# Kernel tuning notes

Measured on AMD Instinct MI355X. Metric: run time of the kernel, lower is better.

The kernel has to match this reference:

```python
import jax, jax.numpy as jnp
import numpy as np

DT = 0.001          # continuous-dynamics step (dt > 0 branch)
KERNEL_SIZE = 16384 # L
P, H = 1024, 256    # d_state, d_input (= d_output)


def setup_inputs() -> dict:
    key = jax.random.key(0)
    kAr, kAi, kB, kC = jax.random.split(key, 4)
    # Continuous diagonal state matrix: real part in [strong, weak] = [-0.5, -0.01] (stable),
    # imaginary part uniform in [-pi, pi] (mimics diagonal_state_space_matrix init).
    Ar = jax.random.uniform(kAr, (P,), minval=-0.5, maxval=-0.01)
    Ai = jax.random.uniform(kAi, (P,), minval=-np.pi, maxval=np.pi)
    A = jnp.stack([Ar, Ai], axis=-1).astype(jnp.float32)            # (P, 2) view_as_real
    # B, C ~ uniform disk (radius 1): scaled complex gaussians are a fine stand-in numerically.
    B = (jax.random.normal(kB, (P, H, 2)) / np.sqrt(H)).astype(jnp.float32)   # (P, H, 2)
    C = (jax.random.normal(kC, (H, P, 2)) / np.sqrt(P)).astype(jnp.float32)   # (H, P, 2)
    return {"A": A, "B": B, "C": C}


def _as_complex(x):
    return x[..., 0] + 1j * x[..., 1]


def reference(A, B, C):
    """Vandermonde SSM kernel generation (continuous dt > 0 branch).
    Returns kernel (H, L, 2) = real view of complex kernel (H, L)."""
    Ac = _as_complex(A)   # (P,) complex
    Bc = _as_complex(B)   # (P, H)
    Cc = _as_complex(C)   # (H, P)

    # ZOH-style discretization
    A_bar = jnp.exp(Ac * DT)                               # (P,)
    B_bar = ((A_bar - 1.0) / Ac)[:, None] * Bc             # (P, H)

    # Vandermonde matrix V[p, l] = A_bar[p] ** l  (complex power == exp(l * log(a)))
    powers = jnp.arange(KERNEL_SIZE, dtype=jnp.float32)    # (L,)
    V = jnp.exp(jnp.log(A_bar)[:, None] * powers[None, :]) # (P, L)

    # W[h, p] = C[h, p] * B_bar[p, h]; kernel[h, l] = sum_p W[h, p] * V[p, l]
    W = Cc * B_bar.T                                       # (H, P)
    kernel = jnp.einsum('hp,pl->hl', W, V)                 # (H, L) complex
    return jnp.stack([kernel.real, kernel.imag], axis=-1)  # (H, L, 2) float32
```

## Files before the change

kernel.cpp:

```cpp
#include <hip/hip_runtime.h>
#include <hip/hip_fp16.h>

#define P_DIM 1024
#define H_DIM 256
#define L_DIM 16384
#define DT 0.001f
#define TWOPI 6.283185307179586f
#define INV2PI 0.15915494309189535f
#define WSCALE 4096.0f
#define INV_WSCALE (1.0f / 4096.0f)
#define BM 128
#define BN 128
#define BK 64
#define NT 256

typedef _Float16 f16x8 __attribute__((ext_vector_type(8)));
typedef float f32x4 __attribute__((ext_vector_type(4)));

#define GPTR(p) (const __attribute__((address_space(1))) unsigned*)(p)
#define LPTR(p) (__attribute__((address_space(3))) unsigned*)(p)

union H2U { __half2 h; unsigned u; };

__device__ __forceinline__ float2 cmulf(float2 a, float2 b) {
    return make_float2(a.x * b.x - a.y * b.y, a.x * b.y + a.y * b.x);
}

__global__ __launch_bounds__(256)
void prep_kernel(const float* __restrict__ Ag, const float* __restrict__ Bg,
                 const float* __restrict__ Cg, __half* __restrict__ W2) {
    __shared__ float2 Bt[64][33];
    __shared__ float2 sc[64];
    const int t  = threadIdx.x;
    const int p0 = (blockIdx.x & 15) << 6;
    const int h0 = (blockIdx.x >> 4) << 5;

    if (t < 64) {
        float2 a = ((const float2*)Ag)[p0 + t];
        float er = __expf(a.x * DT);
        float s, c; __sincosf(a.y * DT, &s, &c);
        float nr = er * c - 1.f, ni = er * s;
        float inv = 1.f / (a.x * a.x + a.y * a.y);
        sc[t] = make_float2((nr * a.x + ni * a.y) * inv, (ni * a.x - nr * a.y) * inv);
    }
    #pragma unroll
    for (int i = 0; i < 8; ++i) {
        int idx = i * 256 + t, p = idx >> 5, h = idx & 31;
        Bt[p][h] = ((const float2*)Bg)[(size_t)(p0 + p) * H_DIM + h0 + h];
    }
    __syncthreads();
    #pragma unroll
    for (int i = 0; i < 8; ++i) {
        int idx = i * 256 + t, h = idx >> 6, p = idx & 63;
        float2 cc = ((const float2*)Cg)[(size_t)(h0 + h) * P_DIM + p0 + p];
        float2 s2 = sc[p], b = Bt[p][h0 ? h : h];
        float2 tv = cmulf(cc, s2);
        float wr = (tv.x * b.x - tv.y * b.y) * WSCALE;
        float wi = (tv.x * b.y + tv.y * b.x) * WSCALE;
        ((__half2*)W2)[(size_t)(h0 + h) * P_DIM + p0 + p] =
            __float22half2_rn(make_float2(wr, wi));
    }
}

__global__ __launch_bounds__(NT, 2)
void vand_mfma_kernel(const float* __restrict__ Ag,
                      const _Float16* __restrict__ W2,
                      float* __restrict__ out) {
    __shared__ __attribute__((aligned(16))) _Float16 As[2][BM * BK];
    __shared__ __attribute__((aligned(16))) _Float16 Bs[2][BN * BK];

    const int tid  = threadIdx.x;
    const int lane = tid & 63;
    const int w    = tid >> 6;
    const int wm   = w & 1, wn = w >> 1;
    const int m0   = blockIdx.y * BM;
    const int nb   = blockIdx.x * BN;
    const int lb   = blockIdx.x * (BN / 2);

    const float2* Ag2 = (const float2*)Ag;

    f32x4 acc[4][4];
    #pragma unroll
    for (int mt = 0; mt < 4; ++mt)
        #pragma unroll
        for (int nt = 0; nt < 4; ++nt)
            acc[mt][nt] = (f32x4){0.f, 0.f, 0.f, 0.f};

    const int q    = tid & 15;
    const int llq  = (tid >> 4) << 2;
    const float l0f = (float)(lb + llq);
    const int grp  = q >> 1, sub = (q & 1) << 2;

    const int goff = (lane >> 3) * 2048 + (((lane & 7) ^ (lane >> 3)) << 3);
    const _Float16* gwbase = W2 + (size_t)(m0 + (w << 5)) * 2048;
    const int ldsoff = (w << 5) * 64;

    _Float16* Acur = &As[0][0]; _Float16* Bcur = &Bs[0][0];
    _Float16* Anxt = &As[1][0]; _Float16* Bnxt = &Bs[1][0];

#define DMA_CHUNK(K0, DST)                                                        \
    {                                                                             \
        const _Float16* gw = gwbase + (K0) + goff;                                \
        _Float16* lB = (DST) + ldsoff;                                            \
        _Pragma("unroll")                                                         \
        for (int r = 0; r < 4; ++r)                                               \
            __builtin_amdgcn_global_load_lds(GPTR(gw + r * 8 * 2048),             \
                                             LPTR(lB + r * 8 * 64), 16, 0, 0);    \
    }

#define VGEN_CHUNK(K0, DST)                                                       \
    {                                                                             \
        float2 a0 = Ag2[((K0) >> 1) + 2 * q];                                     \
        float2 a1 = Ag2[((K0) >> 1) + 2 * q + 1];                                 \
        float c0x = a0.x * DT, c0y = a0.y * (DT * INV2PI);                        \
        float c1x = a1.x * DT, c1y = a1.y * (DT * INV2PI);                        \
        float s, c;                                                               \
        float e0 = __expf(c0x); __sincosf(c0y * TWOPI, &s, &c);                   \
        float2 ab0 = make_float2(e0 * c, e0 * s);                                 \
        float e1 = __expf(c1x); __sincosf(c1y * TWOPI, &s, &c);                   \
        float2 ab1 = make_float2(e1 * c, e1 * s);                                 \
        float mg = __expf(c0x * l0f);                                             \
        float x = c0y * l0f; x -= rintf(x); __sincosf(x * TWOPI, &s, &c);         \
        float2 v0 = make_float2(mg * c, mg * s);                                  \
        mg = __expf(c1x * l0f);                                                   \
        x = c1y * l0f; x -= rintf(x); __sincosf(x * TWOPI, &s, &c);               \
        float2 v1 = make_float2(mg * c, mg * s);                                  \
        _Pragma("unroll")                                                         \
        for (int j = 0; j < 4; ++j) {                                             \
            int n0 = 2 * (llq + j);                                               \
            H2U h0u, h1u, h2u, h3u;                                               \
            h0u.h = __float22half2_rn(make_float2(v0.x, -v0.y));                  \
            h1u.h = __float22half2_rn(make_float2(v1.x, -v1.y));                  \
            h2u.h = __float22half2_rn(make_float2(v0.y, v0.x));                   \
            h3u.h = __float22half2_rn(make_float2(v1.y, v1.x));                   \
            int e0i = n0 * 64 + ((grp ^ (n0 & 7)) << 3) + sub;                    \
            int e1i = (n0 + 1) * 64 + ((grp ^ ((n0 + 1) & 7)) << 3) + sub;        \
            *(uint2*)((DST) + e0i) = make_uint2(h0u.u, h1u.u);                    \
            *(uint2*)((DST) + e1i) = make_uint2(h2u.u, h3u.u);                    \
            if (j < 3) { v0 = cmulf(v0, ab0); v1 = cmulf(v1, ab1); }              \
        }                                                                         \
    }

    DMA_CHUNK(0, Acur)
    VGEN_CHUNK(0, Bcur)
    __syncthreads();

    for (int kk = 0; kk < 32; ++kk) {
        if (kk < 31) {
            const int k1 = (kk + 1) * BK;
            DMA_CHUNK(k1, Anxt)
            VGEN_CHUNK(k1, Bnxt)
        }
        #pragma unroll
        for (int ks = 0; ks < 2; ++ks) {
            f16x8 af[4], bf[4];
            const int g = ks * 4 + (lane >> 4);
            #pragma unroll
            for (int t = 0; t < 4; ++t) {
                int m = wm * 64 + t * 16 + (lane & 15);
                af[t] = *(const f16x8*)(Acur + m * 64 + ((g ^ (m & 7)) << 3));
                int n = wn * 64 + t * 16 + (lane & 15);
                bf[t] = *(const f16x8*)(Bcur + n * 64 + ((g ^ (n & 7)) << 3));
            }
            #pragma unroll
            for (int mt = 0; mt < 4; ++mt)
                #pragma unroll
                for (int nt = 0; nt < 4; ++nt)
                    acc[mt][nt] = __builtin_amdgcn_mfma_f32_16x16x32_f16(
                        af[mt], bf[nt], acc[mt][nt], 0, 0, 0);
        }
        __syncthreads();
        _Float16* tA = Acur; Acur = Anxt; Anxt = tA;
        _Float16* tB = Bcur; Bcur = Bnxt; Bnxt = tB;
    }

    #pragma unroll
    for (int mt = 0; mt < 4; ++mt) {
        #pragma unroll
        for (int nt = 0; nt < 4; ++nt) {
            int h = m0 + wm * 64 + mt * 16 + ((lane >> 4) << 2);
            int n = nb + wn * 64 + nt * 16 + (lane & 15);
            #pragma unroll
            for (int r = 0; r < 4; ++r)
                out[(size_t)(h + r) * 32768 + n] = acc[mt][nt][r] * INV_WSCALE;
        }
    }
#undef DMA_CHUNK
#undef VGEN_CHUNK
}

extern "C" void kernel_launch(void* const* d_in, const int* in_sizes, int n_in,
                              void* d_out, int out_size, void* d_ws, size_t ws_size,
                              hipStream_t stream) {
    const float* A = (const float*)d_in[0];
    const float* B = (const float*)d_in[1];
    const float* C = (const float*)d_in[2];
    float* out = (float*)d_out;
    __half* W2 = (__half*)d_ws;

    prep_kernel<<<dim3(128), dim3(256), 0, stream>>>(A, B, C, W2);
    vand_mfma_kernel<<<dim3(L_DIM * 2 / BN, H_DIM / BM), dim3(NT), 0, stream>>>(
        A, (const _Float16*)W2, out);
}
```

Before: 111.7 us.

## Precompute discretized A table in LDS and regenerate Vandermonde tile with padded layout

The discretized A_bar values are now computed once per block into a shared-memory table, so each Vandermonde chunk no longer recomputes exp/sincos for the step factor. Thread mapping changes so each thread handles one state pair over 8 consecutive positions, halving the per-chunk transcendental starting-point evaluations. The B tile switches from XOR swizzle to a padded row stride with 4-byte stores. In exchange, the longer recurrence chain of 7 complex multiplies adds fp16 error and extra LDS, and the padded layout may bring bank conflicts on the stores.

Result: no change. 109.6 us (-1.9%).

```diff
diff --git a/kernel.cpp b/kernel.cpp
--- a/kernel.cpp
+++ b/kernel.cpp
@@ -13,6 +13,7 @@
 #define BN 128
 #define BK 64
 #define NT 256
+#define LDB 72
 
 typedef _Float16 f16x8 __attribute__((ext_vector_type(8)));
 typedef float f32x4 __attribute__((ext_vector_type(4)));
@@ -53,7 +54,7 @@
     for (int i = 0; i < 8; ++i) {
         int idx = i * 256 + t, h = idx >> 6, p = idx & 63;
         float2 cc = ((const float2*)Cg)[(size_t)(h0 + h) * P_DIM + p0 + p];
-        float2 s2 = sc[p], b = Bt[p][h0 ? h : h];
+        float2 s2 = sc[p], b = Bt[p][h];
         float2 tv = cmulf(cc, s2);
         float wr = (tv.x * b.x - tv.y * b.y) * WSCALE;
         float wi = (tv.x * b.y + tv.y * b.x) * WSCALE;
@@ -67,7 +68,8 @@
                       const _Float16* __restrict__ W2,
                       float* __restrict__ out) {
     __shared__ __attribute__((aligned(16))) _Float16 As[2][BM * BK];
-    __shared__ __attribute__((aligned(16))) _Float16 Bs[2][BN * BK];
+    __shared__ __attribute__((aligned(16))) _Float16 Bs[2][BN * LDB];
+    __shared__ float2 Atab[P_DIM];
 
     const int tid  = threadIdx.x;
     const int lane = tid & 63;
@@ -79,6 +81,15 @@
 
     const float2* Ag2 = (const float2*)Ag;
 
+    #pragma unroll
+    for (int i = 0; i < 4; ++i) {
+        int p = tid + i * 256;
+        float2 a = Ag2[p];
+        float e = __expf(a.x * DT);
+        float s, c; __sincosf(a.y * DT, &s, &c);
+        Atab[p] = make_float2(e * c, e * s);
+    }
+
     f32x4 acc[4][4];
     #pragma unroll
     for (int mt = 0; mt < 4; ++mt)
@@ -86,10 +97,10 @@
         for (int nt = 0; nt < 4; ++nt)
             acc[mt][nt] = (f32x4){0.f, 0.f, 0.f, 0.f};
 
-    const int q    = tid & 15;
-    const int llq  = (tid >> 4) << 2;
-    const float l0f = (float)(lb + llq);
-    const int grp  = q >> 1, sub = (q & 1) << 2;
+    const int pl    = tid & 31;
+    const int lg    = tid >> 5;
+    const float l0f = (float)(lb + lg * 8);
+    const int bpbase = lg * 16 * LDB + 2 * pl;
 
     const int goff = (lane >> 3) * 2048 + (((lane & 7) ^ (lane >> 3)) << 3);
     const _Float16* gwbase = W2 + (size_t)(m0 + (w << 5)) * 2048;
@@ -110,37 +121,27 @@
 
 #define VGEN_CHUNK(K0, DST)                                                       \
     {                                                                             \
-        float2 a0 = Ag2[((K0) >> 1) + 2 * q];                                     \
-        float2 a1 = Ag2[((K0) >> 1) + 2 * q + 1];                                 \
-        float c0x = a0.x * DT, c0y = a0.y * (DT * INV2PI);                        \
-        float c1x = a1.x * DT, c1y = a1.y * (DT * INV2PI);                        \
-        float s, c;                                                               \
-        float e0 = __expf(c0x); __sincosf(c0y * TWOPI, &s, &c);                   \
-        float2 ab0 = make_float2(e0 * c, e0 * s);                                 \
-        float e1 = __expf(c1x); __sincosf(c1y * TWOPI, &s, &c);                   \
-        float2 ab1 = make_float2(e1 * c, e1 * s);                                 \
-        float mg = __expf(c0x * l0f);                                             \
-        float x = c0y * l0f; x -= rintf(x); __sincosf(x * TWOPI, &s, &c);         \
-        float2 v0 = make_float2(mg * c, mg * s);                                  \
-        mg = __expf(c1x * l0f);                                                   \
-        x = c1y * l0f; x -= rintf(x); __sincosf(x * TWOPI, &s, &c);               \
-        float2 v1 = make_float2(mg * c, mg * s);                                  \
+        const int pg = ((K0) >> 1) + pl;                                          \
+        float2 a  = Ag2[pg];                                                      \
+        float2 ab = Atab[pg];                                                     \
+        float cx = a.x * DT, cy = a.y * (DT * INV2PI);                            \
+        float mg = __expf(cx * l0f);                                              \
+        float x  = cy * l0f; x -= rintf(x);                                       \
+        float s, c; __sincosf(x * TWOPI, &s, &c);                                 \
+        float2 v = make_float2(mg * c, mg * s);                                   \
+        _Float16* bp = (DST) + bpbase;                                            \
         _Pragma("unroll")                                                         \
-        for (int j = 0; j < 4; ++j) {                                             \
-            int n0 = 2 * (llq + j);                                               \
-            H2U h0u, h1u, h2u, h3u;                                               \
-            h0u.h = __float22half2_rn(make_float2(v0.x, -v0.y));                  \
-            h1u.h = __float22half2_rn(make_float2(v1.x, -v1.y));                  \
-            h2u.h = __float22half2_rn(make_float2(v0.y, v0.x));                   \
-            h3u.h = __float22half2_rn(make_float2(v1.y, v1.x));                   \
-            int e0i = n0 * 64 + ((grp ^ (n0 & 7)) << 3) + sub;                    \
-            int e1i = (n0 + 1) * 64 + ((grp ^ ((n0 + 1) & 7)) << 3) + sub;        \
-            *(uint2*)((DST) + e0i) = make_uint2(h0u.u, h1u.u);                    \
-            *(uint2*)((DST) + e1i) = make_uint2(h2u.u, h3u.u);                    \
-            if (j < 3) { v0 = cmulf(v0, ab0); v1 = cmulf(v1, ab1); }              \
+        for (int j = 0; j < 8; ++j) {                                             \
+            H2U u0, u1;                                                           \
+            u0.h = __float22half2_rn(make_float2(v.x, -v.y));                     \
+            u1.h = __float22half2_rn(make_float2(v.y, v.x));                      \
+            *(unsigned*)(bp + j * 2 * LDB)       = u0.u;                          \
+            *(unsigned*)(bp + j * 2 * LDB + LDB) = u1.u;                          \
+            if (j < 7) v = cmulf(v, ab);                                          \
         }                                                                         \
     }
 
+    __syncthreads();
     DMA_CHUNK(0, Acur)
     VGEN_CHUNK(0, Bcur)
     __syncthreads();
@@ -160,7 +161,7 @@
                 int m = wm * 64 + t * 16 + (lane & 15);
                 af[t] = *(const f16x8*)(Acur + m * 64 + ((g ^ (m & 7)) << 3));
                 int n = wn * 64 + t * 16 + (lane & 15);
-                bf[t] = *(const f16x8*)(Bcur + n * 64 + ((g ^ (n & 7)) << 3));
+                bf[t] = *(const f16x8*)(Bcur + n * LDB + (g << 3));
             }
             #pragma unroll
             for (int mt = 0; mt < 4; ++mt)
```

## Load W operands directly into registers and precompute A_bar table in LDS

Applied to the files above, without the earlier changes.

The W (A-operand) tile is no longer staged through LDS via global_load_lds. Each wave now loads its MFMA fragments straight from global memory into double-buffered registers, prefetching one k-step ahead. A per-block LDS table of A_bar, scaled log-magnitude and phase is built once, which removes the repeated exp/sincos of A in every chunk. The loop is unrolled by two with explicit barriers and s_setprio around the MFMAs. This trades LDS traffic and transcendental work for more VGPRs and uncoalesced global loads, which risks occupancy at launch bound 2.

Result: slower. 131.3 us (+17.5%).

```diff
diff --git a/kernel.cpp b/kernel.cpp
--- a/kernel.cpp
+++ b/kernel.cpp
@@ -17,9 +17,6 @@
 typedef _Float16 f16x8 __attribute__((ext_vector_type(8)));
 typedef float f32x4 __attribute__((ext_vector_type(4)));
 
-#define GPTR(p) (const __attribute__((address_space(1))) unsigned*)(p)
-#define LPTR(p) (__attribute__((address_space(3))) unsigned*)(p)
-
 union H2U { __half2 h; unsigned u; };
 
 __device__ __forceinline__ float2 cmulf(float2 a, float2 b) {
@@ -53,7 +50,7 @@
     for (int i = 0; i < 8; ++i) {
         int idx = i * 256 + t, h = idx >> 6, p = idx & 63;
         float2 cc = ((const float2*)Cg)[(size_t)(h0 + h) * P_DIM + p0 + p];
-        float2 s2 = sc[p], b = Bt[p][h0 ? h : h];
+        float2 s2 = sc[p], b = Bt[p][h];
         float2 tv = cmulf(cc, s2);
         float wr = (tv.x * b.x - tv.y * b.y) * WSCALE;
         float wi = (tv.x * b.y + tv.y * b.x) * WSCALE;
@@ -66,8 +63,8 @@
 void vand_mfma_kernel(const float* __restrict__ Ag,
                       const _Float16* __restrict__ W2,
                       float* __restrict__ out) {
-    __shared__ __attribute__((aligned(16))) _Float16 As[2][BM * BK];
     __shared__ __attribute__((aligned(16))) _Float16 Bs[2][BN * BK];
+    __shared__ float4 Atab[P_DIM];
 
     const int tid  = threadIdx.x;
     const int lane = tid & 63;
@@ -79,6 +76,15 @@
 
     const float2* Ag2 = (const float2*)Ag;
 
+    #pragma unroll
+    for (int i = 0; i < 4; ++i) {
+        int p = tid + i * 256;
+        float2 a = Ag2[p];
+        float e = __expf(a.x * DT);
+        float s, c; __sincosf(a.y * DT, &s, &c);
+        Atab[p] = make_float4(e * c, e * s, a.x * DT, a.y * (DT * INV2PI));
+    }
+
     f32x4 acc[4][4];
     #pragma unroll
     for (int mt = 0; mt < 4; ++mt)
@@ -91,39 +97,32 @@
     const float l0f = (float)(lb + llq);
     const int grp  = q >> 1, sub = (q & 1) << 2;
 
-    const int goff = (lane >> 3) * 2048 + (((lane & 7) ^ (lane >> 3)) << 3);
-    const _Float16* gwbase = W2 + (size_t)(m0 + (w << 5)) * 2048;
-    const int ldsoff = (w << 5) * 64;
-
-    _Float16* Acur = &As[0][0]; _Float16* Bcur = &Bs[0][0];
-    _Float16* Anxt = &As[1][0]; _Float16* Bnxt = &Bs[1][0];
-
-#define DMA_CHUNK(K0, DST)                                                        \
+    const _Float16* gw0 = W2 + (size_t)(m0 + wm * 64 + (lane & 15)) * 2048
+                              + ((lane >> 4) << 3);
+
+    f16x8 wA[2][4], wB[2][4];
+
+#define WLOAD(K0, R)                                                              \
     {                                                                             \
-        const _Float16* gw = gwbase + (K0) + goff;                                \
-        _Float16* lB = (DST) + ldsoff;                                            \
+        const _Float16* g = gw0 + (K0);                                           \
         _Pragma("unroll")                                                         \
-        for (int r = 0; r < 4; ++r)                                               \
-            __builtin_amdgcn_global_load_lds(GPTR(gw + r * 8 * 2048),             \
-                                             LPTR(lB + r * 8 * 64), 16, 0, 0);    \
+        for (int ks = 0; ks < 2; ++ks)                                            \
+            _Pragma("unroll")                                                     \
+            for (int t = 0; t < 4; ++t)                                           \
+                R[ks][t] = *(const f16x8*)(g + t * 32768 + ks * 32);              \
     }
 
 #define VGEN_CHUNK(K0, DST)                                                       \
     {                                                                             \
-        float2 a0 = Ag2[((K0) >> 1) + 2 * q];                                     \
-        float2 a1 = Ag2[((K0) >> 1) + 2 * q + 1];                                 \
-        float c0x = a0.x * DT, c0y = a0.y * (DT * INV2PI);                        \
-        float c1x = a1.x * DT, c1y = a1.y * (DT * INV2PI);                        \
+        const int pg = ((K0) >> 1) + 2 * q;                                       \
+        float4 t0 = Atab[pg], t1 = Atab[pg + 1];                                  \
+        float2 ab0 = make_float2(t0.x, t0.y), ab1 = make_float2(t1.x, t1.y);      \
         float s, c;                                                               \
-        float e0 = __expf(c0x); __sincosf(c0y * TWOPI, &s, &c);                   \
-        float2 ab0 = make_float2(e0 * c, e0 * s);                                 \
-        float e1 = __expf(c1x); __sincosf(c1y * TWOPI, &s, &c);                   \
-        float2 ab1 = make_float2(e1 * c, e1 * s);                                 \
-        float mg = __expf(c0x * l0f);                                             \
-        float x = c0y * l0f; x -= rintf(x); __sincosf(x * TWOPI, &s, &c);         \
+        float mg = __expf(t0.z * l0f);                                            \
+        float x  = t0.w * l0f; x -= rintf(x); __sincosf(x * TWOPI, &s, &c);       \
         float2 v0 = make_float2(mg * c, mg * s);                                  \
-        mg = __expf(c1x * l0f);                                                   \
-        x = c1y * l0f; x -= rintf(x); __sincosf(x * TWOPI, &s, &c);               \
+        mg = __expf(t1.z * l0f);                                                  \
+        x  = t1.w * l0f; x -= rintf(x); __sincosf(x * TWOPI, &s, &c);             \
         float2 v1 = make_float2(mg * c, mg * s);                                  \
         _Pragma("unroll")                                                         \
         for (int j = 0; j < 4; ++j) {                                             \
@@ -133,45 +132,66 @@
             h1u.h = __float22half2_rn(make_float2(v1.x, -v1.y));                  \
             h2u.h = __float22half2_rn(make_float2(v0.y, v0.x));                   \
             h3u.h = __float22half2_rn(make_float2(v1.y, v1.x));                   \
-            int e0i = n0 * 64 + ((grp ^ (n0 & 7)) << 3) + sub;                    \
-            int e1i = (n0 + 1) * 64 + ((grp ^ ((n0 + 1) & 7)) << 3) + sub;        \
-            *(uint2*)((DST) + e0i) = make_uint2(h0u.u, h1u.u);                    \
-            *(uint2*)((DST) + e1i) = make_uint2(h2u.u, h3u.u);                    \
+            int e0 = n0 * 64 + ((grp ^ (n0 & 7)) << 3) + sub;                     \
+            int e1 = (n0 + 1) * 64 + ((grp ^ ((n0 + 1) & 7)) << 3) + sub;         \
+            *(uint2*)((DST) + e0) = make_uint2(h0u.u, h1u.u);                     \
+            *(uint2*)((DST) + e1) = make_uint2(h2u.u, h3u.u);                     \
             if (j < 3) { v0 = cmulf(v0, ab0); v1 = cmulf(v1, ab1); }              \
         }                                                                         \
     }
 
-    DMA_CHUNK(0, Acur)
-    VGEN_CHUNK(0, Bcur)
+#define MFMA_PHASE(WREG, BUF)                                                     \
+    {                                                                             \
+        _Pragma("unroll")                                                         \
+        for (int ks = 0; ks < 2; ++ks) {                                          \
+            f16x8 bf[4];                                                          \
+            const int g = ks * 4 + (lane >> 4);                                   \
+            _Pragma("unroll")                                                     \
+            for (int t = 0; t < 4; ++t) {                                         \
+                int n = wn * 64 + t * 16 + (lane & 15);                           \
+                bf[t] = *(const f16x8*)((BUF) + n * 64 + ((g ^ (n & 7)) << 3));   \
+            }                                                                     \
+            __builtin_amdgcn_s_setprio(1);                                        \
+            _Pragma("unroll")                                                     \
+            for (int mt = 0; mt < 4; ++mt)                                        \
+                _Pragma("unroll")                                                 \
+                for (int nt = 0; nt < 4; ++nt)                                    \
+                    acc[mt][nt] = __builtin_amdgcn_mfma_f32_16x16x32_f16(         \
+                        WREG[ks][mt], bf[nt], acc[mt][nt], 0, 0, 0);              \
+            __builtin_amdgcn_s_setprio(0);                                        \
+        }                                                                         \
+    }
+
+#define PUBLISH                                                                   \
+    asm volatile("s_waitcnt lgkmcnt(0)" ::: "memory");                            \
+    __builtin_amdgcn_sched_barrier(0);                                            \
+    __builtin_amdgcn_s_barrier();                                                 \
+    __builtin_amdgcn_sched_barrier(0);
+
+#define BOTBAR                                                                    \
+    __builtin_amdgcn_sched_barrier(0);                                            \
+    __builtin_amdgcn_s_barrier();                                                 \
+    __builtin_amdgcn_sched_barrier(0);
+
     __syncthreads();
-
-    for (int kk = 0; kk < 32; ++kk) {
-        if (kk < 31) {
-            const int k1 = (kk + 1) * BK;
-            DMA_CHUNK(k1, Anxt)
-            VGEN_CHUNK(k1, Bnxt)
+    WLOAD(0, wA)
+    VGEN_CHUNK(0, &Bs[0][0])
+    PUBLISH
+
+    for (int kk = 0; kk < 32; kk += 2) {
+        WLOAD((kk + 1) * BK, wB)
+        VGEN_CHUNK((kk + 1) * BK, &Bs[1][0])
+        PUBLISH
+        MFMA_PHASE(wA, &Bs[0][0])
+        BOTBAR
+        {
+            const int kn = (kk + 2 < 32) ? (kk + 2) : 31;
+            WLOAD(kn * BK, wA)
+            if (kk + 2 < 32) VGEN_CHUNK((kk + 2) * BK, &Bs[0][0])
         }
-        #pragma unroll
-        for (int ks = 0; ks < 2; ++ks) {
-            f16x8 af[4], bf[4];
-            const int g = ks * 4 + (lane >> 4);
-            #pragma unroll
-            for (int t = 0; t < 4; ++t) {
-                int m = wm * 64 + t * 16 + (lane & 15);
-                af[t] = *(const f16x8*)(Acur + m * 64 + ((g ^ (m & 7)) << 3));
-                int n = wn * 64 + t * 16 + (lane & 15);
-                bf[t] = *(const f16x8*)(Bcur + n * 64 + ((g ^ (n & 7)) << 3));
-            }
-            #pragma unroll
-            for (int mt = 0; mt < 4; ++mt)
-                #pragma unroll
-                for (int nt = 0; nt < 4; ++nt)
-                    acc[mt][nt] = __builtin_amdgcn_mfma_f32_16x16x32_f16(
-                        af[mt], bf[nt], acc[mt][nt], 0, 0, 0);
-        }
-        __syncthreads();
-        _Float16* tA = Acur; Acur = Anxt; Anxt = tA;
-        _Float16* tB = Bcur; Bcur = Bnxt; Bnxt = tB;
+        PUBLISH
+        MFMA_PHASE(wB, &Bs[1][0])
+        BOTBAR
     }
 
     #pragma unroll
@@ -185,8 +205,11 @@
                 out[(size_t)(h + r) * 32768 + n] = acc[mt][nt][r] * INV_WSCALE;
         }
     }
-#undef DMA_CHUNK
+#undef WLOAD
 #undef VGEN_CHUNK
+#undef MFMA_PHASE
+#undef PUBLISH
+#undef BOTBAR
 }
 
 extern "C" void kernel_launch(void* const* d_in, const int* in_sizes, int n_in,
```

## Split block into producer and MFMA consumer waves with shared A table

Applied to the files above, without the earlier changes.

Doubles the block to 512 threads and specialises waves: four producer waves issue the W DMA and generate the Vandermonde tile into the next LDS buffer, while four consumer waves run the MFMA loop with raised priority on the current buffer. A per-block LDS table of discretized A values (A_bar, scaled log terms) replaces the repeated per-chunk exp/sincos of A_bar. The aim is to overlap V generation and loads with matrix math instead of serialising them in every wave. In exchange, MFMA work is concentrated on half the waves, there is extra LDS for the table, and explicit waitcnts plus raw barriers add synchronisation points each iteration.

Measured after the change: 108.6 us. -2.7%, faster.

```diff
diff --git a/kernel.cpp b/kernel.cpp
--- a/kernel.cpp
+++ b/kernel.cpp
@@ -12,7 +12,7 @@
 #define BM 128
 #define BN 128
 #define BK 64
-#define NT 256
+#define NT 512
 
 typedef _Float16 f16x8 __attribute__((ext_vector_type(8)));
 typedef float f32x4 __attribute__((ext_vector_type(4)));
@@ -53,7 +53,7 @@
     for (int i = 0; i < 8; ++i) {
         int idx = i * 256 + t, h = idx >> 6, p = idx & 63;
         float2 cc = ((const float2*)Cg)[(size_t)(h0 + h) * P_DIM + p0 + p];
-        float2 s2 = sc[p], b = Bt[p][h0 ? h : h];
+        float2 s2 = sc[p], b = Bt[p][h];
         float2 tv = cmulf(cc, s2);
         float wr = (tv.x * b.x - tv.y * b.y) * WSCALE;
         float wi = (tv.x * b.y + tv.y * b.x) * WSCALE;
@@ -62,22 +62,43 @@
     }
 }
 
-__global__ __launch_bounds__(NT, 2)
+__global__ __launch_bounds__(NT, 4)
 void vand_mfma_kernel(const float* __restrict__ Ag,
                       const _Float16* __restrict__ W2,
                       float* __restrict__ out) {
     __shared__ __attribute__((aligned(16))) _Float16 As[2][BM * BK];
     __shared__ __attribute__((aligned(16))) _Float16 Bs[2][BN * BK];
+    __shared__ float4 Atab[P_DIM];
 
     const int tid  = threadIdx.x;
     const int lane = tid & 63;
     const int w    = tid >> 6;
-    const int wm   = w & 1, wn = w >> 1;
+    const bool producer = (w < 4);
     const int m0   = blockIdx.y * BM;
     const int nb   = blockIdx.x * BN;
     const int lb   = blockIdx.x * (BN / 2);
 
     const float2* Ag2 = (const float2*)Ag;
+
+    #pragma unroll
+    for (int i = 0; i < 2; ++i) {
+        int p = tid + i * 512;
+        float2 a = Ag2[p];
+        float e = __expf(a.x * DT);
+        float s, c; __sincosf(a.y * DT, &s, &c);
+        Atab[p] = make_float4(e * c, e * s, a.x * DT, a.y * (DT * INV2PI));
+    }
+
+    const int q    = tid & 15;
+    const int llq  = (tid >> 4) << 2;
+    const float l0f = (float)(lb + llq);
+    const int grp  = q >> 1, sub = (q & 1) << 2;
+    const int goff = (lane >> 3) * 2048 + (((lane & 7) ^ (lane >> 3)) << 3);
+    const _Float16* gwbase = W2 + (size_t)(m0 + (w << 5)) * 2048;
+    const int ldsoff = (w << 5) * 64;
+
+    const int wc = w - 4;
+    const int wm = wc & 1, wn = wc >> 1;
 
     f32x4 acc[4][4];
     #pragma unroll
@@ -85,15 +106,6 @@
         #pragma unroll
         for (int nt = 0; nt < 4; ++nt)
             acc[mt][nt] = (f32x4){0.f, 0.f, 0.f, 0.f};
-
-    const int q    = tid & 15;
-    const int llq  = (tid >> 4) << 2;
-    const float l0f = (float)(lb + llq);
-    const int grp  = q >> 1, sub = (q & 1) << 2;
-
-    const int goff = (lane >> 3) * 2048 + (((lane & 7) ^ (lane >> 3)) << 3);
-    const _Float16* gwbase = W2 + (size_t)(m0 + (w << 5)) * 2048;
-    const int ldsoff = (w << 5) * 64;
 
     _Float16* Acur = &As[0][0]; _Float16* Bcur = &Bs[0][0];
     _Float16* Anxt = &As[1][0]; _Float16* Bnxt = &Bs[1][0];
@@ -110,20 +122,15 @@
 
 #define VGEN_CHUNK(K0, DST)                                                       \
     {                                                                             \
-        float2 a0 = Ag2[((K0) >> 1) + 2 * q];                                     \
-        float2 a1 = Ag2[((K0) >> 1) + 2 * q + 1];                                 \
-        float c0x = a0.x * DT, c0y = a0.y * (DT * INV2PI);                        \
-        float c1x = a1.x * DT, c1y = a1.y * (DT * INV2PI);                        \
+        const int pg = ((K0) >> 1) + 2 * q;                                       \
+        float4 t0 = Atab[pg], t1 = Atab[pg + 1];                                  \
+        float2 ab0 = make_float2(t0.x, t0.y), ab1 = make_float2(t1.x, t1.y);      \
         float s, c;                                                               \
-        float e0 = __expf(c0x); __sincosf(c0y * TWOPI, &s, &c);                   \
-        float2 ab0 = make_float2(e0 * c, e0 * s);                                 \
-        float e1 = __expf(c1x); __sincosf(c1y * TWOPI, &s, &c);                   \
-        float2 ab1 = make_float2(e1 * c, e1 * s);                                 \
-        float mg = __expf(c0x * l0f);                                             \
-        float x = c0y * l0f; x -= rintf(x); __sincosf(x * TWOPI, &s, &c);         \
+        float mg = __expf(t0.z * l0f);                                            \
+        float x  = t0.w * l0f; x -= rintf(x); __sincosf(x * TWOPI, &s, &c);       \
         float2 v0 = make_float2(mg * c, mg * s);                                  \
-        mg = __expf(c1x * l0f);                                                   \
-        x = c1y * l0f; x -= rintf(x); __sincosf(x * TWOPI, &s, &c);               \
+        mg = __expf(t1.z * l0f);                                                  \
+        x  = t1.w * l0f; x -= rintf(x); __sincosf(x * TWOPI, &s, &c);             \
         float2 v1 = make_float2(mg * c, mg * s);                                  \
         _Pragma("unroll")                                                         \
         for (int j = 0; j < 4; ++j) {                                             \
@@ -133,56 +140,72 @@
             h1u.h = __float22half2_rn(make_float2(v1.x, -v1.y));                  \
             h2u.h = __float22half2_rn(make_float2(v0.y, v0.x));                   \
             h3u.h = __float22half2_rn(make_float2(v1.y, v1.x));                   \
-            int e0i = n0 * 64 + ((grp ^ (n0 & 7)) << 3) + sub;                    \
-            int e1i = (n0 + 1) * 64 + ((grp ^ ((n0 + 1) & 7)) << 3) + sub;        \
-            *(uint2*)((DST) + e0i) = make_uint2(h0u.u, h1u.u);                    \
-            *(uint2*)((DST) + e1i) = make_uint2(h2u.u, h3u.u);                    \
+            int e0 = n0 * 64 + ((grp ^ (n0 & 7)) << 3) + sub;                     \
+            int e1 = (n0 + 1) * 64 + ((grp ^ ((n0 + 1) & 7)) << 3) + sub;         \
+            *(uint2*)((DST) + e0) = make_uint2(h0u.u, h1u.u);                     \
+            *(uint2*)((DST) + e1) = make_uint2(h2u.u, h3u.u);                     \
             if (j < 3) { v0 = cmulf(v0, ab0); v1 = cmulf(v1, ab1); }              \
         }                                                                         \
     }
 
-    DMA_CHUNK(0, Acur)
-    VGEN_CHUNK(0, Bcur)
     __syncthreads();
+    if (producer) {
+        DMA_CHUNK(0, Acur)
+        VGEN_CHUNK(0, Bcur)
+        asm volatile("s_waitcnt vmcnt(0) lgkmcnt(0)" ::: "memory");
+    }
+    __builtin_amdgcn_sched_barrier(0);
+    __builtin_amdgcn_s_barrier();
+    __builtin_amdgcn_sched_barrier(0);
 
     for (int kk = 0; kk < 32; ++kk) {
-        if (kk < 31) {
-            const int k1 = (kk + 1) * BK;
-            DMA_CHUNK(k1, Anxt)
-            VGEN_CHUNK(k1, Bnxt)
+        if (producer) {
+            if (kk < 31) {
+                DMA_CHUNK((kk + 1) * BK, Anxt)
+                VGEN_CHUNK((kk + 1) * BK, Bnxt)
+                asm volatile("s_waitcnt vmcnt(0) lgkmcnt(0)" ::: "memory");
+            }
+        } else {
+            #pragma unroll
+            for (int ks = 0; ks < 2; ++ks) {
+                f16x8 af[4], bf[4];
+                const int g = ks * 4 + (lane >> 4);
+                #pragma unroll
+                for (int t = 0; t < 4; ++t) {
+                    int m = wm * 64 + t * 16 + (lane & 15);
+                    af[t] = *(const f16x8*)(Acur + m * 64 + ((g ^ (m & 7)) << 3));
+                    int n = wn * 64 + t * 16 + (lane & 15);
+                    bf[t] = *(const f16x8*)(Bcur + n * 64 + ((g ^ (n & 7)) << 3));
+                }
+                __builtin_amdgcn_s_setprio(1);
+                #pragma unroll
+                for (int mt = 0; mt < 4; ++mt)
+                    #pragma unroll
+                    for (int nt = 0; nt < 4; ++nt)
+                        acc[mt][nt] = __builtin_amdgcn_mfma_f32_16x16x32_f16(
+                            af[mt], bf[nt], acc[mt][nt], 0, 0, 0);
+                __builtin_amdgcn_s_setprio(0);
+            }
         }
-        #pragma unroll
-        for (int ks = 0; ks < 2; ++ks) {
-            f16x8 af[4], bf[4];
-            const int g = ks * 4 + (lane >> 4);
-            #pragma unroll
-            for (int t = 0; t < 4; ++t) {
-                int m = wm * 64 + t * 16 + (lane & 15);
-                af[t] = *(const f16x8*)(Acur + m * 64 + ((g ^ (m & 7)) << 3));
-                int n = wn * 64 + t * 16 + (lane & 15);
-                bf[t] = *(const f16x8*)(Bcur + n * 64 + ((g ^ (n & 7)) << 3));
-            }
-            #pragma unroll
-            for (int mt = 0; mt < 4; ++mt)
-                #pragma unroll
-                for (int nt = 0; nt < 4; ++nt)
-                    acc[mt][nt] = __builtin_amdgcn_mfma_f32_16x16x32_f16(
-                        af[mt], bf[nt], acc[mt][nt], 0, 0, 0);
-        }
-        __syncthreads();
+        __builtin_amdgcn_sched_barrier(0);
+        __builtin_amdgcn_s_barrier();
+        __builtin_amdgcn_sched_barrier(0);
+
         _Float16* tA = Acur; Acur = Anxt; Anxt = tA;
         _Float16* tB = Bcur; Bcur = Bnxt; Bnxt = tB;
     }
 
-    #pragma unroll
-    for (int mt = 0; mt < 4; ++mt) {
+    if (!producer) {
         #pragma unroll
-        for (int nt = 0; nt < 4; ++nt) {
-            int h = m0 + wm * 64 + mt * 16 + ((lane >> 4) << 2);
-            int n = nb + wn * 64 + nt * 16 + (lane & 15);
+        for (int mt = 0; mt < 4; ++mt) {
             #pragma unroll
-            for (int r = 0; r < 4; ++r)
-                out[(size_t)(h + r) * 32768 + n] = acc[mt][nt][r] * INV_WSCALE;
+            for (int nt = 0; nt < 4; ++nt) {
+                int h = m0 + wm * 64 + mt * 16 + ((lane >> 4) << 2);
+                int n = nb + wn * 64 + nt * 16 + (lane & 15);
+                #pragma unroll
+                for (int r = 0; r < 4; ++r)
+                    out[(size_t)(h + r) * 32768 + n] = acc[mt][nt][r] * INV_WSCALE;
+            }
         }
     }
 #undef DMA_CHUNK
```
